# Kernel tuning notes

Measured on AMD Instinct MI355X. Metric: run time of the kernel, lower is better.

The kernel has to match this reference:

```python
import jax, jax.numpy as jnp
import numpy as np

N = 100000      # num nodes
E = 1600000     # num edges
B = 256         # num graphs in batch
D_IN = 128
H = 256
BN_EPS = 1e-5


def setup_inputs() -> dict:
    key = jax.random.key(0)
    ks = jax.random.split(key, 16)
    inp = {}
    inp["x"] = jax.random.normal(ks[0], (N, D_IN), jnp.float32)
    inp["edge_index"] = jax.random.randint(ks[1], (2, E), 0, N, jnp.int32)
    inp["edge_weight"] = jax.random.uniform(ks[2], (E,), jnp.float32)
    inp["batch"] = jnp.sort(jax.random.randint(ks[3], (N,), 0, B, jnp.int32))
    # GCN layer 1
    inp["W1"] = jax.random.normal(ks[4], (D_IN, H), jnp.float32) * 0.05
    inp["b1"] = jnp.zeros((H,), jnp.float32)
    inp["g1"] = jnp.ones((H,), jnp.float32)
    inp["be1"] = jnp.zeros((H,), jnp.float32)
    inp["rm1"] = jnp.zeros((H,), jnp.float32)
    inp["rv1"] = jnp.ones((H,), jnp.float32)
    # GCN layer 2
    inp["W2"] = jax.random.normal(ks[5], (H, H), jnp.float32) * 0.05
    inp["b2"] = jnp.zeros((H,), jnp.float32)
    inp["g2"] = jnp.ones((H,), jnp.float32)
    inp["be2"] = jnp.zeros((H,), jnp.float32)
    inp["rm2"] = jnp.zeros((H,), jnp.float32)
    inp["rv2"] = jnp.ones((H,), jnp.float32)
    # classifier: Linear(256,256)+BN, Linear(256,128)+BN, Linear(128,2)
    inp["cW1"] = jax.random.normal(ks[6], (H, 256), jnp.float32) * 0.05
    inp["cb1"] = jnp.zeros((256,), jnp.float32)
    inp["cg1"] = jnp.ones((256,), jnp.float32)
    inp["cbe1"] = jnp.zeros((256,), jnp.float32)
    inp["crm1"] = jnp.zeros((256,), jnp.float32)
    inp["crv1"] = jnp.ones((256,), jnp.float32)
    inp["cW2"] = jax.random.normal(ks[7], (256, 128), jnp.float32) * 0.05
    inp["cb2"] = jnp.zeros((128,), jnp.float32)
    inp["cg2"] = jnp.ones((128,), jnp.float32)
    inp["cbe2"] = jnp.zeros((128,), jnp.float32)
    inp["crm2"] = jnp.zeros((128,), jnp.float32)
    inp["crv2"] = jnp.ones((128,), jnp.float32)
    inp["cW3"] = jax.random.normal(ks[8], (128, 2), jnp.float32) * 0.05
    inp["cb3"] = jnp.zeros((2,), jnp.float32)
    return inp


def _bn(x, g, b, rm, rv):
    # eval-mode BatchNorm1d with running stats
    return (x - rm) * jax.lax.rsqrt(rv + BN_EPS) * g + b


def _gcn_conv(x, W, b, src, dst, ew):
    # PyG GCNConv: add self-loops (weight 1), symmetric normalization
    deg = jax.ops.segment_sum(ew, dst, num_segments=N) + 1.0  # incl. self loop
    dinv = jnp.where(deg > 0, jax.lax.rsqrt(deg), 0.0)        # [N]
    h = x @ W                                                  # [N, out]
    norm = dinv[src] * ew * dinv[dst]                          # [E]
    agg = jax.ops.segment_sum(h[src] * norm[:, None], dst, num_segments=N)
    agg = agg + h * (dinv * dinv)[:, None]                     # self-loop term
    return agg + b


def _forward(x, edge_index, edge_weight, batch,
             W1, b1, g1, be1, rm1, rv1,
             W2, b2, g2, be2, rm2, rv2,
             cW1, cb1, cg1, cbe1, crm1, crv1,
             cW2, cb2, cg2, cbe2, crm2, crv2,
             cW3, cb3):
    src, dst = edge_index[0], edge_index[1]
    # layer 0 (no residual: i == 0)
    h = jax.nn.relu(_bn(_gcn_conv(x, W1, b1, src, dst, edge_weight), g1, be1, rm1, rv1))
    res = h
    # layer 1 (residual: dims match, i > 0); dropout = identity (eval)
    h = jax.nn.relu(_bn(_gcn_conv(h, W2, b2, src, dst, edge_weight), g2, be2, rm2, rv2))
    h = h + res
    # global mean pool per graph
    cnt = jax.ops.segment_sum(jnp.ones((N,), x.dtype), batch, num_segments=B)
    emb = jax.ops.segment_sum(h, batch, num_segments=B) / jnp.maximum(cnt, 1.0)[:, None]
    # classifier MLP
    z = jax.nn.relu(_bn(emb @ cW1 + cb1, cg1, cbe1, crm1, crv1))
    z = jax.nn.relu(_bn(z @ cW2 + cb2, cg2, cbe2, crm2, crv2))
    logits = z @ cW3 + cb3
    return logits, emb


def reference(x, edge_index, edge_weight, batch,
              W1, b1, g1, be1, rm1, rv1,
              W2, b2, g2, be2, rm2, rv2,
              cW1, cb1, cg1, cbe1, crm1, crv1,
              cW2, cb2, cg2, cbe2, crm2, crv2,
              cW3, cb3):
    return _forward(x, edge_index, edge_weight, batch,
                    W1, b1, g1, be1, rm1, rv1,
                    W2, b2, g2, be2, rm2, rv2,
                    cW1, cb1, cg1, cbe1, crm1, crv1,
                    cW2, cb2, cg2, cbe2, crm2, crv2,
                    cW3, cb3)
```

## Files before the change

### kernel.cpp

```cpp
#include <hip/hip_runtime.h>
#include <stdint.h>

#define NN 100000
#define NE 1600000
#define NB 256
#define DIN 128
#define HH 256
#define BN_EPS 1e-5f

typedef unsigned short bf16_t;
typedef __attribute__((ext_vector_type(8))) short short8;
typedef __attribute__((ext_vector_type(4))) short short4v;
typedef __attribute__((ext_vector_type(4))) float f32x4;
typedef __attribute__((ext_vector_type(2))) float f32x2;

struct __align__(8) EPair { int c; float v; };

#define DEG_MASK ((1ULL << 40) - 1ULL)
#define DEG_ONE  (1ULL << 40)
#define FXS 1048576.0f

__device__ __forceinline__ float bf2f(unsigned short u) {
    union { unsigned int i; float f; } v;
    v.i = ((unsigned int)u) << 16;
    return v.f;
}
__device__ __forceinline__ bf16_t f2bf(float f) {
    union { float f; unsigned int i; } v;
    v.f = f;
    unsigned int x = v.i;
    return (bf16_t)((x + 0x7fffu + ((x >> 16) & 1u)) >> 16);
}
__device__ __forceinline__ float ldp(const void* b, int i, int f) {
    return f ? ((const float*)b)[i] : bf2f(((const unsigned short*)b)[i]);
}
__device__ __forceinline__ int dflag_from(const void* rv) {
    return ((((const unsigned int*)rv)[0] & 0xffffu) == 0u) ? 1 : 0;
}

__device__ __forceinline__ void fmadd_row8p(f32x2* acc2, uint2 w, float v) {
#if defined(__HIP_DEVICE_COMPILE__)
    f32x2 vv = {v, v};
    acc2[0] += __builtin_amdgcn_cvt_pk_f32_fp8((int)w.x, false) * vv;
    acc2[1] += __builtin_amdgcn_cvt_pk_f32_fp8((int)w.x, true)  * vv;
    acc2[2] += __builtin_amdgcn_cvt_pk_f32_fp8((int)w.y, false) * vv;
    acc2[3] += __builtin_amdgcn_cvt_pk_f32_fp8((int)w.y, true)  * vv;
#else
    (void)acc2; (void)w; (void)v;
#endif
}
__device__ __forceinline__ unsigned char enc_fp8(float v) {
#if defined(__HIP_DEVICE_COMPILE__)
    int pk = __builtin_amdgcn_cvt_pk_fp8_f32(v, v, 0, false);
    return (unsigned char)(pk & 0xff);
#else
    (void)v; return 0;
#endif
}
__device__ __forceinline__ unsigned int pack4_fp8(float a, float b, float c, float d) {
#if defined(__HIP_DEVICE_COMPILE__)
    int w = __builtin_amdgcn_cvt_pk_fp8_f32(a, b, 0, false);
    w = __builtin_amdgcn_cvt_pk_fp8_f32(c, d, w, true);
    return (unsigned int)w;
#else
    (void)a; (void)b; (void)c; (void)d; return 0;
#endif
}

__device__ __forceinline__ void pack_one(const void* __restrict__ W, bf16_t* __restrict__ P,
                                         int S, int idx, int f) {
    int lane = idx & 63;
    int ts = idx >> 6;
    int s = ts % S;
    int t = ts / S;
    int q = lane >> 4, m = lane & 15;
    int colbase = t * 16 + m;
    int krow = 32 * s + 8 * q;
#pragma unroll
    for (int j = 0; j < 8; j++) P[idx * 8 + j] = f2bf(ldp(W, (krow + j) * 256 + colbase, f));
}

__global__ __launch_bounds__(256) void prep_kernel(const void* __restrict__ x, unsigned int* __restrict__ xc8,
                                                   const void* __restrict__ ew,
                                                   const int* __restrict__ dst,
                                                   const int* __restrict__ batch,
                                                   unsigned long long* __restrict__ cd8,
                                                   unsigned char* __restrict__ occ,
                                                   int* __restrict__ gcount,
                                                   const void* __restrict__ W1, bf16_t* __restrict__ P1,
                                                   const void* __restrict__ W2, bf16_t* __restrict__ P2,
                                                   const void* __restrict__ rv) {
    int i = blockIdx.x * blockDim.x + threadIdx.x;
    int stride = gridDim.x * blockDim.x;
    int shard = blockIdx.x & 7;
    int f = dflag_from(rv);
    if (i < 12288) {
        if (i < 4096) pack_one(W1, P1, 4, i, f);
        else          pack_one(W2, P2, 8, i - 4096, f);
    }
    if (f) {
        const float4* xs = (const float4*)x;
        for (int j = i; j < NN * DIN / 4; j += stride) {
            float4 w = xs[j];
            xc8[j] = pack4_fp8(w.x, w.y, w.z, w.w);
        }
    } else {
        const uint2* xs = (const uint2*)x;
        for (int j = i; j < NN * DIN / 4; j += stride) {
            uint2 w = xs[j];
            xc8[j] = pack4_fp8(bf2f((unsigned short)(w.x & 0xffffu)), bf2f((unsigned short)(w.x >> 16)),
                               bf2f((unsigned short)(w.y & 0xffffu)), bf2f((unsigned short)(w.y >> 16)));
        }
    }
    for (int j = i; j < NE; j += stride) {
        float w = ldp(ew, j, f);
        int d = dst[j];
        unsigned long long wfx = (unsigned long long)(unsigned int)(w * FXS + 0.5f);
        unsigned long long old = atomicAdd(&cd8[(size_t)shard * NN + d], DEG_ONE | wfx);
        occ[j] = (unsigned char)(old >> 40);
    }
    int lane = threadIdx.x & 63;
    for (int j = i; j < NN; j += stride) {
        int b = batch[j];
        bool boundary = (lane == 0) || (j == 0) || (batch[j - 1] != b);
        unsigned long long bmask = __ballot(boundary);
        bool islast = (lane == 63) || (j + 1 >= NN) || (batch[j + 1] != b);
        if (islast) {
            unsigned long long below = bmask & ((lane == 63) ? ~0ull : ((1ull << (lane + 1)) - 1ull));
            int first = 63 - __builtin_clzll(below);
            atomicAdd(&gcount[b], lane - first + 1);
        }
    }
}

#define SCAN_NB ((NN + 1023) / 1024)

__global__ __launch_bounds__(1024) void scanA(const unsigned long long* __restrict__ cd8,
                                              int* __restrict__ rowptr,
                                              float* __restrict__ dinv,
                                              int* __restrict__ bsum) {
    __shared__ int wsum[16];
    int tid = threadIdx.x, lane = tid & 63, wid = tid >> 6;
    int i = blockIdx.x * 1024 + tid;
    int v = 0;
    if (i < NN) {
        float wf = 0.f;
#pragma unroll
        for (int k = 0; k < 8; k++) {
            unsigned long long cv = cd8[(size_t)k * NN + i];
            v += (int)(cv >> 40);
            wf += (float)(cv & DEG_MASK);
        }
        dinv[i] = rsqrtf(wf * (1.0f / FXS) + 1.0f);
    }
    int sc = v;
#pragma unroll
    for (int off = 1; off < 64; off <<= 1) {
        int t = __shfl_up(sc, off, 64);
        if (lane >= off) sc += t;
    }
    if (lane == 63) wsum[wid] = sc;
    __syncthreads();
    if (wid == 0 && lane < 16) {
        int ws = wsum[lane];
        int scw = ws;
#pragma unroll
        for (int off = 1; off < 16; off <<= 1) {
            int t = __shfl_up(scw, off, 64);
            if (lane >= off) scw += t;
        }
        if (lane == 15) bsum[blockIdx.x] = scw;
        wsum[lane] = scw - ws;
    }
    __syncthreads();
    if (i < NN) rowptr[i] = wsum[wid] + sc - v;
}

__global__ __launch_bounds__(64) void scanB(int* __restrict__ bsum, int* __restrict__ rowptr,
                                            const int* __restrict__ gcount, int* __restrict__ gptr) {
    int lane = threadIdx.x;
    {
        int i0 = lane * 2;
        int v0 = (i0 < SCAN_NB) ? bsum[i0] : 0;
        int v1 = (i0 + 1 < SCAN_NB) ? bsum[i0 + 1] : 0;
        int tsum = v0 + v1;
        int sc = tsum;
#pragma unroll
        for (int off = 1; off < 64; off <<= 1) {
            int t = __shfl_up(sc, off, 64);
            if (lane >= off) sc += t;
        }
        int excl = sc - tsum;
        if (i0 < SCAN_NB) bsum[i0] = excl;
        if (i0 + 1 < SCAN_NB) bsum[i0 + 1] = excl + v0;
        if (lane == 63) rowptr[NN] = sc;
    }
    {
        int i0 = lane * 4;
        int v0 = gcount[i0], v1 = gcount[i0 + 1], v2 = gcount[i0 + 2], v3 = gcount[i0 + 3];
        int tsum = v0 + v1 + v2 + v3;
        int sc = tsum;
#pragma unroll
        for (int off = 1; off < 64; off <<= 1) {
            int t = __shfl_up(sc, off, 64);
            if (lane >= off) sc += t;
        }
        int excl = sc - tsum;
        gptr[i0] = excl;
        gptr[i0 + 1] = excl + v0;
        gptr[i0 + 2] = excl + v0 + v1;
        gptr[i0 + 3] = excl + v0 + v1 + v2;
        if (lane == 63) gptr[256] = sc;
    }
}

__global__ __launch_bounds__(1024) void scanC(int* __restrict__ rowptr, const int* __restrict__ bsum,
                                              const unsigned long long* __restrict__ cd8,
                                              int* __restrict__ offs) {
    int i = blockIdx.x * 1024 + threadIdx.x;
    if (i < NN) {
        int rp = rowptr[i] + bsum[blockIdx.x];
        rowptr[i] = rp;
        int cum = rp;
#pragma unroll
        for (int k = 0; k < 8; k++) {
            offs[(size_t)k * NN + i] = cum;
            cum += (int)(cd8[(size_t)k * NN + i] >> 40);
        }
    }
}

__global__ __launch_bounds__(256) void scatter_kernel(const int* __restrict__ src,
                                                      const int* __restrict__ dst,
                                                      const void* __restrict__ ew,
                                                      const float* __restrict__ dinv,
                                                      const int* __restrict__ offs,
                                                      const unsigned char* __restrict__ occ,
                                                      EPair* __restrict__ ep,
                                                      const void* __restrict__ rv) {
    int i = blockIdx.x * blockDim.x + threadIdx.x;
    int f = dflag_from(rv);
    int shard = blockIdx.x & 7;
    if (i < NE) {
        int s = src[i], d = dst[i];
        float nv = dinv[s] * ldp(ew, i, f) * dinv[d];
        int pos = offs[(size_t)shard * NN + d] + occ[i];
        EPair pr;
        pr.c = s;
        pr.v = nv;
        ep[pos] = pr;
    }
}

template <int K, bool WRITE_OUT, bool ACCUM>
__global__ __launch_bounds__(256, 6) void fused_layer(
        const void* __restrict__ Xv,
        const bf16_t* __restrict__ P,
        const int* __restrict__ rowptr,
        const EPair* __restrict__ ep,
        const float* __restrict__ dinv,
        const int* __restrict__ batch,
        const void* __restrict__ bias,
        const void* __restrict__ gam,
        const void* __restrict__ bet,
        const void* __restrict__ rmean,
        const void* __restrict__ rvar,
        void* __restrict__ outbuf,
        float* __restrict__ partial,
        float* __restrict__ partial2,
        float* __restrict__ embf) {
    constexpr int S = K / 32;
    constexpr int ROWELL = K + 8;
    constexpr int LPR = K / 8;
    constexpr int EDG = 64 / LPR;
    constexpr int UN = 8;
    constexpr int BE = EDG * UN;
    __shared__ __align__(16) bf16_t T[16 * ROWELL];
    const char* Xb = (const char*)Xv;
    int fl = dflag_from(rvar);
    int widx = threadIdx.x >> 6;
    int lane = threadIdx.x & 63;
    int h = lane / LPR;
    int l = lane % LPR;
    int f0 = l * 8;
    int rowbase = blockIdx.x * 16;

    int rp = rowptr[rowbase + (lane < 17 ? lane : 16)];
    float dvv = dinv[rowbase + (lane < 16 ? lane : 15)];

    int j0 = widx * 4;
    EPair win = ep[__shfl(rp, j0) + lane];
    for (int j = 0; j < 4; j++) {
        int r = j0 + j;
        int e0 = __shfl(rp, r);
        int e1 = __shfl(rp, r + 1);
        int n = e1 - e0;
        float di = __shfl(dvv, r);
        int node = rowbase + r;
        EPair nxtwin = ep[e1 + lane];
        f32x2 acc2[4];
#pragma unroll
        for (int c = 0; c < 4; c++) acc2[c] = (f32x2){0.f, 0.f};
        EPair cw = win;
        uint2 wself = *(const uint2*)(Xb + (size_t)node * K + l * 8);
        if (n <= BE) {
            uint2 wreg[UN];
            float vreg[UN];
#pragma unroll
            for (int u = 0; u < UN; u++) {
                int idx = EDG * u + h;
                bool ok = idx < n;
                int sl = ok ? idx : 0;
                int c = __shfl(cw.c, sl);
                float v = __shfl(cw.v, sl);
                wreg[u] = *(const uint2*)(Xb + (size_t)(ok ? c : node) * K + l * 8);
                vreg[u] = ok ? v : 0.f;
            }
#pragma unroll
            for (int u = 0; u < UN; u++) fmadd_row8p(acc2, wreg[u], vreg[u]);
        } else {
            int base = 0;
            while (base < n) {
                int winend = n - base;
                if (winend > 64) winend = 64;
                for (int s0 = 0; s0 < winend; s0 += BE) {
                    uint2 wreg[UN];
                    float vreg[UN];
#pragma unroll
                    for (int u = 0; u < UN; u++) {
                        int idx = s0 + EDG * u + h;
                        bool ok = idx < winend;
                        int sl = ok ? idx : 0;
                        int c = __shfl(cw.c, sl);
                        float v = __shfl(cw.v, sl);
                        wreg[u] = *(const uint2*)(Xb + (size_t)(ok ? c : node) * K + l * 8);
                        vreg[u] = ok ? v : 0.f;
                    }
#pragma unroll
                    for (int u = 0; u < UN; u++) fmadd_row8p(acc2, wreg[u], vreg[u]);
                }
                base += winend;
                if (base < n) cw = ep[e0 + base + lane];
            }
        }
        fmadd_row8p(acc2, wself, (h == 0) ? di * di : 0.f);
        float acc[8];
#pragma unroll
        for (int c = 0; c < 4; c++) { acc[2 * c] = acc2[c][0]; acc[2 * c + 1] = acc2[c][1]; }
#pragma unroll
        for (int d = LPR; d < 64; d <<= 1) {
#pragma unroll
            for (int c = 0; c < 8; c++) acc[c] += __shfl_xor(acc[c], d);
        }
        if (h == 0) {
            short8 o;
#pragma unroll
            for (int c = 0; c < 8; c++) o[c] = (short)f2bf(acc[c]);
            *(short8*)&T[r * ROWELL + f0] = o;
        }
        win = nxtwin;
    }
    __syncthreads();

    int m = lane & 15, q = lane >> 4;
    f32x4 acc16[4];
#pragma unroll
    for (int tt = 0; tt < 4; tt++) acc16[tt] = (f32x4){0.f, 0.f, 0.f, 0.f};
#pragma unroll
    for (int s = 0; s < S; s++) {
        short8 af = *(const short8*)&T[m * ROWELL + 32 * s + 8 * q];
#pragma unroll
        for (int tt = 0; tt < 4; tt++) {
            int t = j0 + tt;
            short8 bfr = *(const short8*)(P + ((size_t)(t * S + s) * 64 + lane) * 8);
            acc16[tt] = __builtin_amdgcn_mfma_f32_16x16x32_bf16(af, bfr, acc16[tt], 0, 0, 0);
        }
    }
    if (WRITE_OUT) __syncthreads();
    unsigned char* T8 = (unsigned char*)T;

    int g0 = batch[rowbase];
    int g15 = batch[rowbase + 15];
    int rg[4];
#pragma unroll
    for (int r = 0; r < 4; r++) rg[r] = batch[rowbase + q * 4 + r];
#pragma unroll
    for (int tt = 0; tt < 4; tt++) {
        int col = (j0 + tt) * 16 + m;
        float a = rsqrtf(ldp(rvar, col, fl) + BN_EPS) * ldp(gam, col, fl);
        float bc = (ldp(bias, col, fl) - ldp(rmean, col, fl)) * a + ldp(bet, col, fl);
        float cs0 = 0.f, cs1 = 0.f;
#pragma unroll
        for (int r = 0; r < 4; r++) {
            int row = q * 4 + r;
            float v = fmaxf(acc16[tt][r] * a + bc, 0.f);
            if (WRITE_OUT) T8[row * 256 + col] = enc_fp8(v);
            if (rg[r] == g0) cs0 += v;
            else if (rg[r] == g15) cs1 += v;
            else atomicAdd(&embf[(size_t)rg[r] * 256 + col], v);
        }
        cs0 += __shfl_xor(cs0, 16, 64);
        cs0 += __shfl_xor(cs0, 32, 64);
        cs1 += __shfl_xor(cs1, 16, 64);
        cs1 += __shfl_xor(cs1, 32, 64);
        if (q == 0) {
            size_t pidx = (size_t)blockIdx.x * 256 + col;
            partial[pidx]  = (ACCUM ? partial[pidx]  : 0.f) + cs0;
            partial2[pidx] = (ACCUM ? partial2[pidx] : 0.f) + cs1;
        }
    }
    if (WRITE_OUT) {
        __syncthreads();
        int tid = threadIdx.x;
        uint4 wv = *(const uint4*)&T8[tid * 16];
        *(uint4*)((char*)outbuf + (size_t)rowbase * 256 + tid * 16) = wv;
    }
}

__global__ __launch_bounds__(256) void classifier_kernel(const float* __restrict__ partial,
                                                         const float* __restrict__ partial2,
                                                         const int* __restrict__ gptr,
                                                         const float* __restrict__ embf,
                                                         const void* cW1, const void* cb1,
                                                         const void* cg1, const void* cbe1,
                                                         const void* crm1, const void* crv1,
                                                         const void* cW2, const void* cb2,
                                                         const void* cg2, const void* cbe2,
                                                         const void* crm2, const void* crv2,
                                                         const void* cW3, const void* cb3,
                                                         void* __restrict__ d_out) {
    int g = blockIdx.x, tid = threadIdx.x;
    int fl = dflag_from(crv1);
    __shared__ float se[256];
    __shared__ float z1[256];
    __shared__ float z2[128];
    int s = gptr[g], e = gptr[g + 1];
    float acc = embf[g * 256 + tid];
    int blo = (s + 15) >> 4, bhi = (e + 15) >> 4;
    for (int b = blo; b < bhi; b++) acc += partial[(size_t)b * 256 + tid];
    int bs = s >> 4;
    if ((s & 15) && (16 * bs + 15) < e) acc += partial2[(size_t)bs * 256 + tid];
    float mval = acc / fmaxf((float)(e - s), 1.f);
    se[tid] = mval;
    if (fl) ((float*)d_out)[512 + g * 256 + tid] = mval;
    else    ((bf16_t*)d_out)[512 + g * 256 + tid] = f2bf(mval);
    __syncthreads();
    {
        float sm = 0.f;
#pragma unroll 8
        for (int k = 0; k < 256; k++) sm += se[k] * ldp(cW1, k * 256 + tid, fl);
        sm += ldp(cb1, tid, fl);
        sm = (sm - ldp(crm1, tid, fl)) * rsqrtf(ldp(crv1, tid, fl) + BN_EPS) * ldp(cg1, tid, fl) + ldp(cbe1, tid, fl);
        z1[tid] = fmaxf(sm, 0.f);
    }
    __syncthreads();
    if (tid < 128) {
        float sm = 0.f;
#pragma unroll 8
        for (int k = 0; k < 256; k++) sm += z1[k] * ldp(cW2, k * 128 + tid, fl);
        sm += ldp(cb2, tid, fl);
        sm = (sm - ldp(crm2, tid, fl)) * rsqrtf(ldp(crv2, tid, fl) + BN_EPS) * ldp(cg2, tid, fl) + ldp(cbe2, tid, fl);
        z2[tid] = fmaxf(sm, 0.f);
    }
    __syncthreads();
    if (tid < 2) {
        float sm = 0.f;
        for (int k = 0; k < 128; k++) sm += z2[k] * ldp(cW3, k * 2 + tid, fl);
        sm += ldp(cb3, tid, fl);
        if (fl) ((float*)d_out)[g * 2 + tid] = sm;
        else    ((bf16_t*)d_out)[g * 2 + tid] = f2bf(sm);
    }
}

extern "C" void kernel_launch(void* const* d_in, const int* in_sizes, int n_in,
                              void* d_out, int out_size, void* d_ws, size_t ws_size,
                              hipStream_t stream) {
    const void* x    = d_in[0];
    const int*  eidx = (const int*)d_in[1];
    const void* ew   = d_in[2];
    const int*  batch= (const int*)d_in[3];
    const void* W1   = d_in[4];
    const void* b1   = d_in[5];
    const void* g1   = d_in[6];
    const void* be1  = d_in[7];
    const void* rm1  = d_in[8];
    const void* rv1  = d_in[9];
    const void* W2   = d_in[10];
    const void* b2   = d_in[11];
    const void* g2   = d_in[12];
    const void* be2  = d_in[13];
    const void* rm2  = d_in[14];
    const void* rv2  = d_in[15];
    const void* cW1  = d_in[16];
    const void* cb1  = d_in[17];
    const void* cg1  = d_in[18];
    const void* cbe1 = d_in[19];
    const void* crm1 = d_in[20];
    const void* crv1 = d_in[21];
    const void* cW2  = d_in[22];
    const void* cb2  = d_in[23];
    const void* cg2  = d_in[24];
    const void* cbe2 = d_in[25];
    const void* crm2 = d_in[26];
    const void* crv2 = d_in[27];
    const void* cW3  = d_in[28];
    const void* cb3  = d_in[29];

    const int* src = eidx;
    const int* dst = eidx + NE;

    char* p = (char*)d_ws;
    auto alloc = [&](size_t bytes) -> void* {
        void* r = (void*)p;
        p += (bytes + 255) & ~(size_t)255;
        return r;
    };
    unsigned long long* cd8 = (unsigned long long*)alloc((size_t)8 * NN * 8);
    int*    gcount = (int*)alloc((size_t)NB * 4);
    float*  embf   = (float*)alloc((size_t)NB * 256 * 4);
    size_t zspan = (char*)p - (char*)cd8;
    int*    rowptr = (int*)alloc((size_t)(NN + 1) * 4);
    float*  dinv   = (float*)alloc((size_t)NN * 4);
    int*    bsum   = (int*)alloc((size_t)SCAN_NB * 4);
    int*    gptr   = (int*)alloc((size_t)(NB + 1) * 4);
    int*    offs   = (int*)alloc((size_t)8 * NN * 4);
    unsigned char* occ = (unsigned char*)alloc((size_t)NE);
    float*  partial = (float*)alloc((size_t)(NN / 16) * 256 * 4);
    float*  partial2= (float*)alloc((size_t)(NN / 16) * 256 * 4);
    EPair*  ep     = (EPair*)alloc((size_t)(NE + 64) * 8);
    unsigned int* xc8 = (unsigned int*)alloc((size_t)NN * DIN);
    bf16_t* pW1    = (bf16_t*)alloc((size_t)DIN * 256 * 2);
    bf16_t* pW2    = (bf16_t*)alloc((size_t)256 * 256 * 2);
    void*   hl     = alloc((size_t)NN * 256);

    (void)hipMemsetAsync(cd8, 0, zspan, stream);

    prep_kernel<<<2048, 256, 0, stream>>>(x, xc8, ew, dst, batch, cd8, occ, gcount,
                                          W1, pW1, W2, pW2, rv1);
    scanA<<<SCAN_NB, 1024, 0, stream>>>(cd8, rowptr, dinv, bsum);
    scanB<<<1, 64, 0, stream>>>(bsum, rowptr, gcount, gptr);
    scanC<<<SCAN_NB, 1024, 0, stream>>>(rowptr, bsum, cd8, offs);
    scatter_kernel<<<NE / 256, 256, 0, stream>>>(src, dst, ew, dinv, offs, occ, ep, rv1);

    int blocks = NN / 16;
    fused_layer<128, true, false><<<blocks, 256, 0, stream>>>(
        xc8, pW1, rowptr, ep, dinv, batch, b1, g1, be1, rm1, rv1, hl, partial, partial2, embf);
    fused_layer<256, false, true><<<blocks, 256, 0, stream>>>(
        hl, pW2, rowptr, ep, dinv, batch, b2, g2, be2, rm2, rv2, nullptr, partial, partial2, embf);

    classifier_kernel<<<NB, 256, 0, stream>>>(partial, partial2, gptr, embf,
                                              cW1, cb1, cg1, cbe1, crm1, crv1,
                                              cW2, cb2, cg2, cbe2, crm2, crv2,
                                              cW3, cb3, d_out);
}
```

Before: 495.7 us.

## Restructure neighbor gather into 16-slot batches, raise occupancy, use 32-bit offsets

Replaces the fixed 8-deep unrolled gather with up to four 16-edge batches gated on degree, so low-degree rows issue fewer wasted loads and use fewer registers. Launch bounds change from 6 to 8 waves per SIMD. Address math switches to 32-bit shift-based offsets, and out-of-range lanes read a zero-padded tail written into the edge array by scanB instead of clamping to the self node. Trades load-level parallelism per wave for occupancy, and the padded sentinel entries point at node 0.

```diff
diff --git a/kernel.cpp b/kernel.cpp
--- a/kernel.cpp
+++ b/kernel.cpp
@@ -177,8 +177,11 @@
 }
 
 __global__ __launch_bounds__(64) void scanB(int* __restrict__ bsum, int* __restrict__ rowptr,
-                                            const int* __restrict__ gcount, int* __restrict__ gptr) {
+                                            const int* __restrict__ gcount, int* __restrict__ gptr,
+                                            EPair* __restrict__ ep) {
     int lane = threadIdx.x;
+    EPair pz; pz.c = 0; pz.v = 0.f;
+    ep[NE + lane] = pz;
     {
         int i0 = lane * 2;
         int v0 = (i0 < SCAN_NB) ? bsum[i0] : 0;
@@ -253,7 +256,7 @@
 }
 
 template <int K, bool WRITE_OUT, bool ACCUM>
-__global__ __launch_bounds__(256, 6) void fused_layer(
+__global__ __launch_bounds__(256, 8) void fused_layer(
         const void* __restrict__ Xv,
         const bf16_t* __restrict__ P,
         const int* __restrict__ rowptr,
@@ -273,8 +276,9 @@
     constexpr int ROWELL = K + 8;
     constexpr int LPR = K / 8;
     constexpr int EDG = 64 / LPR;
-    constexpr int UN = 8;
-    constexpr int BE = EDG * UN;
+    constexpr int SLOTB = 16;
+    constexpr int UB = SLOTB / EDG;
+    constexpr int SH = (K == 256) ? 8 : 7;
     __shared__ __align__(16) bf16_t T[16 * ROWELL];
     const char* Xb = (const char*)Xv;
     int fl = dflag_from(rvar);
@@ -283,6 +287,7 @@
     int h = lane / LPR;
     int l = lane % LPR;
     int f0 = l * 8;
+    unsigned loff = (unsigned)(l * 8);
     int rowbase = blockIdx.x * 16;
 
     int rp = rowptr[rowbase + (lane < 17 ? lane : 16)];
@@ -302,47 +307,42 @@
 #pragma unroll
         for (int c = 0; c < 4; c++) acc2[c] = (f32x2){0.f, 0.f};
         EPair cw = win;
-        uint2 wself = *(const uint2*)(Xb + (size_t)node * K + l * 8);
-        if (n <= BE) {
-            uint2 wreg[UN];
-            float vreg[UN];
-#pragma unroll
-            for (int u = 0; u < UN; u++) {
-                int idx = EDG * u + h;
-                bool ok = idx < n;
-                int sl = ok ? idx : 0;
-                int c = __shfl(cw.c, sl);
-                float v = __shfl(cw.v, sl);
-                wreg[u] = *(const uint2*)(Xb + (size_t)(ok ? c : node) * K + l * 8);
-                vreg[u] = ok ? v : 0.f;
-            }
-#pragma unroll
-            for (int u = 0; u < UN; u++) fmadd_row8p(acc2, wreg[u], vreg[u]);
-        } else {
-            int base = 0;
+        uint2 wself = *(const uint2*)(Xb + ((unsigned)node << SH) + loff);
+
+#define GBATCH(B0, LIM) { \
+        uint2 wreg[UB]; \
+        float vreg[UB]; \
+        _Pragma("unroll") \
+        for (int u = 0; u < UB; u++) { \
+            int idx = (B0) + EDG * u + h; \
+            int c = __shfl(cw.c, idx); \
+            float v = __shfl(cw.v, idx); \
+            unsigned off = ((unsigned)c << SH) + loff; \
+            wreg[u] = *(const uint2*)(Xb + off); \
+            vreg[u] = (idx < (LIM)) ? v : 0.f; \
+        } \
+        _Pragma("unroll") \
+        for (int u = 0; u < UB; u++) fmadd_row8p(acc2, wreg[u], vreg[u]); \
+    }
+
+        GBATCH(0, n)
+        if (n > 16) GBATCH(16, n)
+        if (n > 32) GBATCH(32, n)
+        if (n > 48) GBATCH(48, n)
+        if (n > 64) {
+            int base = 64;
+            cw = ep[e0 + base + lane];
             while (base < n) {
                 int winend = n - base;
                 if (winend > 64) winend = 64;
-                for (int s0 = 0; s0 < winend; s0 += BE) {
-                    uint2 wreg[UN];
-                    float vreg[UN];
-#pragma unroll
-                    for (int u = 0; u < UN; u++) {
-                        int idx = s0 + EDG * u + h;
-                        bool ok = idx < winend;
-                        int sl = ok ? idx : 0;
-                        int c = __shfl(cw.c, sl);
-                        float v = __shfl(cw.v, sl);
-                        wreg[u] = *(const uint2*)(Xb + (size_t)(ok ? c : node) * K + l * 8);
-                        vreg[u] = ok ? v : 0.f;
-                    }
-#pragma unroll
-                    for (int u = 0; u < UN; u++) fmadd_row8p(acc2, wreg[u], vreg[u]);
+                for (int s0 = 0; s0 < winend; s0 += SLOTB) {
+                    GBATCH(s0, winend)
                 }
                 base += winend;
                 if (base < n) cw = ep[e0 + base + lane];
             }
         }
+#undef GBATCH
         fmadd_row8p(acc2, wself, (h == 0) ? di * di : 0.f);
         float acc[8];
 #pragma unroll
@@ -538,7 +538,7 @@
     prep_kernel<<<2048, 256, 0, stream>>>(x, xc8, ew, dst, batch, cd8, occ, gcount,
                                           W1, pW1, W2, pW2, rv1);
     scanA<<<SCAN_NB, 1024, 0, stream>>>(cd8, rowptr, dinv, bsum);
-    scanB<<<1, 64, 0, stream>>>(bsum, rowptr, gcount, gptr);
+    scanB<<<1, 64, 0, stream>>>(bsum, rowptr, gcount, gptr, ep);
     scanC<<<SCAN_NB, 1024, 0, stream>>>(rowptr, bsum, cd8, offs);
     scatter_kernel<<<NE / 256, 256, 0, stream>>>(src, dst, ew, dinv, offs, occ, ep, rv1);
 
```

After: 597.9 us. 1.21x slower.
